# Optimization experiments

Hardware: AMD Instinct MI355X
Metric: run time of the kernel (lower is better)

Reference implementation:

```python
import jax, jax.numpy as jnp
import numpy as np

B, NPG, C, DEG, DE = 64, 1024, 512, 32, 16  # graphs, nodes/graph, feat dim, avg degree, edge-feat dim
N = B * NPG
E = N * DEG
RATIO = 0.5


def setup_inputs() -> dict:
    key = jax.random.key(0)
    k1, k2, k3, k4 = jax.random.split(key, 4)
    x = jax.random.normal(k1, (N, C), dtype=jnp.float32)
    # edges drawn within each graph block so batch structure is respected
    local = jax.random.randint(k2, (2, E), 0, NPG, dtype=jnp.int32)
    offsets = jnp.repeat(jnp.arange(B, dtype=jnp.int32) * NPG, NPG * DEG)
    edge_index = local + offsets[None, :]
    edge_attr = jax.random.normal(k3, (E, DE), dtype=jnp.float32)
    batch = jnp.repeat(jnp.arange(B, dtype=jnp.int32), NPG)
    W = jax.random.normal(k4, (C, 1), dtype=jnp.float32) * (1.0 / np.sqrt(C))
    b = jnp.zeros((1,), dtype=jnp.float32)
    return {"x": x, "edge_index": edge_index, "edge_attr": edge_attr, "batch": batch,
            "W": W, "b": b, "num_graphs": B, "nodes_per_graph": NPG}


def _gcn_score(x, edge_index, W, b):
    # PyG GCNConv(in_channels, 1): add self-loops, symmetric D^-1/2 (A+I) D^-1/2 norm
    n = x.shape[0]
    loop = jnp.arange(n, dtype=edge_index.dtype)
    s = jnp.concatenate([edge_index[0], loop])
    d = jnp.concatenate([edge_index[1], loop])
    deg = jnp.zeros((n,), x.dtype).at[d].add(jnp.ones((), x.dtype))  # >= 1 via self loops
    dinv = jax.lax.rsqrt(deg)
    norm = dinv[s] * dinv[d]                       # [E+n]
    h = (x @ W)[:, 0]                               # project first: [n]
    score = jnp.zeros((n,), x.dtype).at[d].add(h[s] * norm) + b[0]
    return score


def reference(x, edge_index, edge_attr, batch, W, b, num_graphs, nodes_per_graph):
    n = x.shape[0]
    k = int(np.ceil(RATIO * nodes_per_graph))
    score = _gcn_score(x, edge_index, W, b)         # [n]
    # per-graph top-k (equal-sized graphs -> fixed-shape top_k over [B, NPG])
    sc = score.reshape(num_graphs, nodes_per_graph)
    _, topi = jax.lax.top_k(sc, k)                  # [B, k], score-descending per graph
    offs = (jnp.arange(num_graphs, dtype=edge_index.dtype) * nodes_per_graph)[:, None]
    perm = (topi.astype(edge_index.dtype) + offs).reshape(-1)  # [B*k]
    x_new = x[perm] * jnp.tanh(score[perm])[:, None]
    batch_new = batch[perm]
    # filter_adj: keep edges with both endpoints selected, remap to new ids.
    # Fixed-shape version: full-length edge list with invalid entries = -1 plus a mask.
    sel = jnp.zeros((n,), bool).at[perm].set(True)
    newidx = jnp.full((n,), -1, edge_index.dtype).at[perm].set(
        jnp.arange(perm.shape[0], dtype=edge_index.dtype))
    src, dst = edge_index[0], edge_index[1]
    edge_mask = sel[src] & sel[dst]                 # [E]
    ei_new = jnp.where(edge_mask[None, :], jnp.stack([newidx[src], newidx[dst]]), -1)
    ea_new = jnp.where(edge_mask[:, None], edge_attr, jnp.zeros((), edge_attr.dtype))
    return x_new, ei_new, ea_new, edge_mask, batch_new, perm
```

## Files before the change

### kernel.cpp

```cpp
#include <hip/hip_runtime.h>
#include <math.h>

#define N_NODES 65536
#define C_DIM   512
#define E_EDGES 2097152
#define DE_DIM  16
#define B_GR    64
#define NPG     1024
#define DEG     32
#define EPG     (NPG * DEG)
#define K_SEL   512
#define NK      (B_GR * K_SEL)

#define OUT_XNEW  0
#define OUT_EI    (NK * C_DIM)
#define OUT_EA    (OUT_EI + 2 * E_EDGES)
#define OUT_MASK  (OUT_EA + (size_t)E_EDGES * DE_DIM)
#define OUT_BATCH (OUT_MASK + E_EDGES)
#define OUT_PERM  (OUT_BATCH + NK)

__global__ void k_proj(const float* __restrict__ x,
                       const float* __restrict__ W,
                       float* __restrict__ h,
                       int*   __restrict__ newidx) {
    __shared__ float sW[C_DIM];
    const int t = threadIdx.x;
    ((float2*)sW)[t] = ((const float2*)W)[t];
    __syncthreads();

    const int wave = t >> 6, lane = t & 63;
    const int node = blockIdx.x * 4 + wave;
    const float* xr = x + (size_t)node * C_DIM + lane * 8;
    float4 a0 = ((const float4*)xr)[0];
    float4 a1 = ((const float4*)xr)[1];
    const float* wr = sW + lane * 8;
    float s = a0.x * wr[0] + a0.y * wr[1] + a0.z * wr[2] + a0.w * wr[3]
            + a1.x * wr[4] + a1.y * wr[5] + a1.z * wr[6] + a1.w * wr[7];
#pragma unroll
    for (int off = 32; off > 0; off >>= 1) s += __shfl_down(s, off, 64);
    if (lane == 0) h[node] = s;

    const int gid = blockIdx.x * 256 + t;
    if (gid < N_NODES) newidx[gid] = -1;
}

__global__ void __launch_bounds__(1024)
k_score_topk(const int* __restrict__ src,
             const int* __restrict__ dst,
             const float* __restrict__ h,
             const float* __restrict__ b,
             int*   __restrict__ newidx,
             int*   __restrict__ permw,
             float* __restrict__ mult,
             float* __restrict__ out_perm,
             float* __restrict__ out_batch) {
    __shared__ float hs[NPG];
    __shared__ float dg[NPG];
    __shared__ float sc[NPG];
    __shared__ unsigned long long keys[NPG];

    const int g = blockIdx.x, t = threadIdx.x;
    const int ebase = g * EPG;
    const int nbase = g * NPG;

    hs[t] = h[nbase + t];
    dg[t] = 0.0f;
    sc[t] = 0.0f;
    __syncthreads();

    const int4* dst4 = (const int4*)(dst + ebase);
#pragma unroll
    for (int it = 0; it < EPG / 4096; ++it) {
        int4 d4 = dst4[it * 1024 + t];
        atomicAdd(&dg[d4.x & (NPG - 1)], 1.0f);
        atomicAdd(&dg[d4.y & (NPG - 1)], 1.0f);
        atomicAdd(&dg[d4.z & (NPG - 1)], 1.0f);
        atomicAdd(&dg[d4.w & (NPG - 1)], 1.0f);
    }
    __syncthreads();
    dg[t] = rsqrtf(dg[t] + 1.0f);
    __syncthreads();

    const int4* src4 = (const int4*)(src + ebase);
#pragma unroll
    for (int it = 0; it < EPG / 4096; ++it) {
        int4 s4 = src4[it * 1024 + t];
        int4 d4 = dst4[it * 1024 + t];
        int s0 = s4.x & (NPG - 1), d0 = d4.x & (NPG - 1);
        int s1 = s4.y & (NPG - 1), d1 = d4.y & (NPG - 1);
        int s2 = s4.z & (NPG - 1), d2 = d4.z & (NPG - 1);
        int s3 = s4.w & (NPG - 1), d3 = d4.w & (NPG - 1);
        atomicAdd(&sc[d0], hs[s0] * dg[s0] * dg[d0]);
        atomicAdd(&sc[d1], hs[s1] * dg[s1] * dg[d1]);
        atomicAdd(&sc[d2], hs[s2] * dg[s2] * dg[d2]);
        atomicAdd(&sc[d3], hs[s3] * dg[s3] * dg[d3]);
    }
    __syncthreads();

    {
        const float scf = sc[t] + hs[t] * dg[t] * dg[t] + b[0];
        sc[t] = scf;
        const unsigned int bits = __float_as_uint(scf);
        const unsigned int u = bits ^ ((bits & 0x80000000u) ? 0xFFFFFFFFu : 0x80000000u);
        keys[t] = ((unsigned long long)(~u) << 32) | (unsigned int)t;
    }
    __syncthreads();

    for (int k = 2; k <= NPG; k <<= 1) {
        for (int j = k >> 1; j > 0; j >>= 1) {
            if (t < NPG / 2) {
                const int i = ((t & ~(j - 1)) << 1) | (t & (j - 1));
                const int p = i | j;
                const bool asc = (i & k) == 0;
                const unsigned long long a = keys[i], bb = keys[p];
                if ((a > bb) == asc) { keys[i] = bb; keys[p] = a; }
            }
            __syncthreads();
        }
    }

    if (t < K_SEL) {
        const int li   = (int)(keys[t] & 0xFFFFFFFFull);
        const int node = nbase + li;
        const int j    = g * K_SEL + t;
        permw[j]     = node;
        newidx[node] = j;
        mult[j]      = tanhf(sc[li]);
        out_perm[j]  = (float)node;
        out_batch[j] = (float)g;
    }
}

__global__ void k_xnew(const float* __restrict__ x,
                       const float* __restrict__ mult,
                       const int* __restrict__ permw,
                       float* __restrict__ out) {
    const int row = blockIdx.x * 2 + (threadIdx.x >> 7);
    const int c   = (threadIdx.x & 127) * 4;
    const int node = permw[row];
    const float tt = mult[row];
    float4 v = *(const float4*)(x + (size_t)node * C_DIM + c);
    v.x *= tt; v.y *= tt; v.z *= tt; v.w *= tt;
    *(float4*)(out + (size_t)row * C_DIM + c) = v;
}

__global__ void k_edges(const int* __restrict__ src,
                        const int* __restrict__ dst,
                        const float* __restrict__ ea,
                        const int* __restrict__ newidx,
                        float* __restrict__ out_ei,
                        float* __restrict__ out_ea,
                        float* __restrict__ out_mask) {
    const int gid = blockIdx.x * 256 + threadIdx.x;
    const int e = gid >> 2, c = gid & 3;
    if (e >= E_EDGES) return;
    const int s = src[e], d = dst[e];
    const int ns = newidx[s], nd = newidx[d];
    const bool m = (ns >= 0) && (nd >= 0);

    float4 v = make_float4(0.f, 0.f, 0.f, 0.f);
    if (m) v = ((const float4*)ea)[(size_t)e * 4 + c];
    ((float4*)out_ea)[(size_t)e * 4 + c] = v;

    if (c == 0) {
        out_ei[e]           = m ? (float)ns : -1.0f;
        out_ei[E_EDGES + e] = m ? (float)nd : -1.0f;
        out_mask[e]         = m ? 1.0f : 0.0f;
    }
}

extern "C" void kernel_launch(void* const* d_in, const int* in_sizes, int n_in,
                              void* d_out, int out_size, void* d_ws, size_t ws_size,
                              hipStream_t stream) {
    const float* x    = (const float*)d_in[0];
    const int*   ei   = (const int*)d_in[1];
    const float* ea   = (const float*)d_in[2];
    const float* W    = (const float*)d_in[4];
    const float* b    = (const float*)d_in[5];
    const int* src = ei;
    const int* dst = ei + E_EDGES;

    float* out = (float*)d_out;

    float* h      = (float*)d_ws;
    int*   newidx = (int*)(h + N_NODES);
    int*   permw  = newidx + N_NODES;
    float* mult   = (float*)(permw + NK);

    k_proj<<<N_NODES / 4, 256, 0, stream>>>(x, W, h, newidx);
    k_score_topk<<<B_GR, 1024, 0, stream>>>(src, dst, h, b, newidx, permw, mult,
                                            out + OUT_PERM, out + OUT_BATCH);
    k_xnew<<<NK / 2, 256, 0, stream>>>(x, mult, permw, out + OUT_XNEW);
    k_edges<<<(E_EDGES * 4) / 256, 256, 0, stream>>>(src, dst, ea, newidx,
                                                     out + OUT_EI, out + OUT_EA,
                                                     out + OUT_MASK);
}
```

Measured before the change: 516.2 us.

## Split per-graph degree and score scatter across four blocks per graph; merge tail kernels

The single 64-block score/top-k kernel is split into three kernels. Degree counting and score scattering each run with four blocks per graph, accumulating privately in shared memory and then adding into global arrays with atomics. A separate kernel then does the sort. The x_new gather and the edge-filter kernels are also merged into one launch, so both kinds of work share the GPU. This targets low occupancy in the old 64-block kernel, at the cost of extra launches and global atomics.

```diff
diff --git a/kernel.cpp b/kernel.cpp
--- a/kernel.cpp
+++ b/kernel.cpp
@@ -9,6 +9,8 @@
 #define NPG     1024
 #define DEG     32
 #define EPG     (NPG * DEG)
+#define PARTS   4
+#define EPP     (EPG / PARTS)
 #define K_SEL   512
 #define NK      (B_GR * K_SEL)
 
@@ -22,6 +24,8 @@
 __global__ void k_proj(const float* __restrict__ x,
                        const float* __restrict__ W,
                        float* __restrict__ h,
+                       float* __restrict__ score,
+                       float* __restrict__ deg,
                        int*   __restrict__ newidx) {
     __shared__ float sW[C_DIM];
     const int t = threadIdx.x;
@@ -41,65 +45,98 @@
     if (lane == 0) h[node] = s;
 
     const int gid = blockIdx.x * 256 + t;
-    if (gid < N_NODES) newidx[gid] = -1;
+    if (gid < N_NODES) {
+        score[gid]  = 0.0f;
+        deg[gid]    = 1.0f;
+        newidx[gid] = -1;
+    }
 }
 
 __global__ void __launch_bounds__(1024)
-k_score_topk(const int* __restrict__ src,
-             const int* __restrict__ dst,
-             const float* __restrict__ h,
-             const float* __restrict__ b,
-             int*   __restrict__ newidx,
-             int*   __restrict__ permw,
-             float* __restrict__ mult,
-             float* __restrict__ out_perm,
-             float* __restrict__ out_batch) {
+k_deg_part(const int* __restrict__ dst, float* __restrict__ deg) {
+    __shared__ float dgp[NPG];
+    const int bg = blockIdx.x;
+    const int g = bg >> 2, part = bg & 3;
+    const int t = threadIdx.x;
+    dgp[t] = 0.0f;
+    __syncthreads();
+
+    const int4* d4 = (const int4*)(dst + g * EPG + part * EPP);
+    int4 a = d4[t], b = d4[1024 + t];
+    atomicAdd(&dgp[a.x & (NPG - 1)], 1.0f);
+    atomicAdd(&dgp[a.y & (NPG - 1)], 1.0f);
+    atomicAdd(&dgp[a.z & (NPG - 1)], 1.0f);
+    atomicAdd(&dgp[a.w & (NPG - 1)], 1.0f);
+    atomicAdd(&dgp[b.x & (NPG - 1)], 1.0f);
+    atomicAdd(&dgp[b.y & (NPG - 1)], 1.0f);
+    atomicAdd(&dgp[b.z & (NPG - 1)], 1.0f);
+    atomicAdd(&dgp[b.w & (NPG - 1)], 1.0f);
+    __syncthreads();
+
+    atomicAdd(&deg[g * NPG + t], dgp[t]);
+}
+
+__global__ void __launch_bounds__(1024)
+k_score_part(const int* __restrict__ src, const int* __restrict__ dst,
+             const float* __restrict__ h, const float* __restrict__ deg,
+             float* __restrict__ score) {
     __shared__ float hs[NPG];
-    __shared__ float dg[NPG];
-    __shared__ float sc[NPG];
+    __shared__ float di[NPG];
+    __shared__ float scp[NPG];
+    const int bg = blockIdx.x;
+    const int g = bg >> 2, part = bg & 3;
+    const int t = threadIdx.x;
+    const int nbase = g * NPG;
+
+    hs[t]  = h[nbase + t];
+    di[t]  = rsqrtf(deg[nbase + t]);
+    scp[t] = 0.0f;
+    __syncthreads();
+
+    const int4* s4 = (const int4*)(src + g * EPG + part * EPP);
+    const int4* d4 = (const int4*)(dst + g * EPG + part * EPP);
+    int4 sa = s4[t], sb = s4[1024 + t];
+    int4 da = d4[t], db = d4[1024 + t];
+    {
+        int s0 = sa.x & (NPG-1), d0 = da.x & (NPG-1);
+        int s1 = sa.y & (NPG-1), d1 = da.y & (NPG-1);
+        int s2 = sa.z & (NPG-1), d2 = da.z & (NPG-1);
+        int s3 = sa.w & (NPG-1), d3 = da.w & (NPG-1);
+        atomicAdd(&scp[d0], hs[s0] * di[s0] * di[d0]);
+        atomicAdd(&scp[d1], hs[s1] * di[s1] * di[d1]);
+        atomicAdd(&scp[d2], hs[s2] * di[s2] * di[d2]);
+        atomicAdd(&scp[d3], hs[s3] * di[s3] * di[d3]);
+    }
+    {
+        int s0 = sb.x & (NPG-1), d0 = db.x & (NPG-1);
+        int s1 = sb.y & (NPG-1), d1 = db.y & (NPG-1);
+        int s2 = sb.z & (NPG-1), d2 = db.z & (NPG-1);
+        int s3 = sb.w & (NPG-1), d3 = db.w & (NPG-1);
+        atomicAdd(&scp[d0], hs[s0] * di[s0] * di[d0]);
+        atomicAdd(&scp[d1], hs[s1] * di[s1] * di[d1]);
+        atomicAdd(&scp[d2], hs[s2] * di[s2] * di[d2]);
+        atomicAdd(&scp[d3], hs[s3] * di[s3] * di[d3]);
+    }
+    __syncthreads();
+
+    atomicAdd(&score[nbase + t], scp[t]);
+}
+
+__global__ void __launch_bounds__(1024)
+k_topk(const float* __restrict__ score, const float* __restrict__ h,
+       const float* __restrict__ deg, const float* __restrict__ b,
+       int*   __restrict__ newidx, int* __restrict__ permw,
+       float* __restrict__ mult,
+       float* __restrict__ out_perm, float* __restrict__ out_batch) {
+    __shared__ float scs[NPG];
     __shared__ unsigned long long keys[NPG];
-
     const int g = blockIdx.x, t = threadIdx.x;
-    const int ebase = g * EPG;
     const int nbase = g * NPG;
 
-    hs[t] = h[nbase + t];
-    dg[t] = 0.0f;
-    sc[t] = 0.0f;
-    __syncthreads();
-
-    const int4* dst4 = (const int4*)(dst + ebase);
-#pragma unroll
-    for (int it = 0; it < EPG / 4096; ++it) {
-        int4 d4 = dst4[it * 1024 + t];
-        atomicAdd(&dg[d4.x & (NPG - 1)], 1.0f);
-        atomicAdd(&dg[d4.y & (NPG - 1)], 1.0f);
-        atomicAdd(&dg[d4.z & (NPG - 1)], 1.0f);
-        atomicAdd(&dg[d4.w & (NPG - 1)], 1.0f);
-    }
-    __syncthreads();
-    dg[t] = rsqrtf(dg[t] + 1.0f);
-    __syncthreads();
-
-    const int4* src4 = (const int4*)(src + ebase);
-#pragma unroll
-    for (int it = 0; it < EPG / 4096; ++it) {
-        int4 s4 = src4[it * 1024 + t];
-        int4 d4 = dst4[it * 1024 + t];
-        int s0 = s4.x & (NPG - 1), d0 = d4.x & (NPG - 1);
-        int s1 = s4.y & (NPG - 1), d1 = d4.y & (NPG - 1);
-        int s2 = s4.z & (NPG - 1), d2 = d4.z & (NPG - 1);
-        int s3 = s4.w & (NPG - 1), d3 = d4.w & (NPG - 1);
-        atomicAdd(&sc[d0], hs[s0] * dg[s0] * dg[d0]);
-        atomicAdd(&sc[d1], hs[s1] * dg[s1] * dg[d1]);
-        atomicAdd(&sc[d2], hs[s2] * dg[s2] * dg[d2]);
-        atomicAdd(&sc[d3], hs[s3] * dg[s3] * dg[d3]);
-    }
-    __syncthreads();
-
     {
-        const float scf = sc[t] + hs[t] * dg[t] * dg[t] + b[0];
-        sc[t] = scf;
+        const float dv  = rsqrtf(deg[nbase + t]);
+        const float scf = score[nbase + t] + h[nbase + t] * dv * dv + b[0];
+        scs[t] = scf;
         const unsigned int bits = __float_as_uint(scf);
         const unsigned int u = bits ^ ((bits & 0x80000000u) ? 0xFFFFFFFFu : 0x80000000u);
         keys[t] = ((unsigned long long)(~u) << 32) | (unsigned int)t;
@@ -125,73 +162,82 @@
         const int j    = g * K_SEL + t;
         permw[j]     = node;
         newidx[node] = j;
-        mult[j]      = tanhf(sc[li]);
+        mult[j]      = tanhf(scs[li]);
         out_perm[j]  = (float)node;
         out_batch[j] = (float)g;
     }
 }
 
-__global__ void k_xnew(const float* __restrict__ x,
+#define EDGE_BLKS (E_EDGES / 64)
+#define XNEW_BLKS (NK / 2)
+
+__global__ void k_tail(const float* __restrict__ x,
                        const float* __restrict__ mult,
                        const int* __restrict__ permw,
-                       float* __restrict__ out) {
-    const int row = blockIdx.x * 2 + (threadIdx.x >> 7);
-    const int c   = (threadIdx.x & 127) * 4;
-    const int node = permw[row];
-    const float tt = mult[row];
-    float4 v = *(const float4*)(x + (size_t)node * C_DIM + c);
-    v.x *= tt; v.y *= tt; v.z *= tt; v.w *= tt;
-    *(float4*)(out + (size_t)row * C_DIM + c) = v;
-}
-
-__global__ void k_edges(const int* __restrict__ src,
-                        const int* __restrict__ dst,
-                        const float* __restrict__ ea,
-                        const int* __restrict__ newidx,
-                        float* __restrict__ out_ei,
-                        float* __restrict__ out_ea,
-                        float* __restrict__ out_mask) {
-    const int gid = blockIdx.x * 256 + threadIdx.x;
-    const int e = gid >> 2, c = gid & 3;
-    if (e >= E_EDGES) return;
-    const int s = src[e], d = dst[e];
-    const int ns = newidx[s], nd = newidx[d];
-    const bool m = (ns >= 0) && (nd >= 0);
-
-    float4 v = make_float4(0.f, 0.f, 0.f, 0.f);
-    if (m) v = ((const float4*)ea)[(size_t)e * 4 + c];
-    ((float4*)out_ea)[(size_t)e * 4 + c] = v;
-
-    if (c == 0) {
-        out_ei[e]           = m ? (float)ns : -1.0f;
-        out_ei[E_EDGES + e] = m ? (float)nd : -1.0f;
-        out_mask[e]         = m ? 1.0f : 0.0f;
+                       const int* __restrict__ src,
+                       const int* __restrict__ dst,
+                       const float* __restrict__ ea,
+                       const int* __restrict__ newidx,
+                       float* __restrict__ out_xnew,
+                       float* __restrict__ out_ei,
+                       float* __restrict__ out_ea,
+                       float* __restrict__ out_mask) {
+    int bid = blockIdx.x;
+    if (bid < EDGE_BLKS) {
+        const int gid = bid * 256 + threadIdx.x;
+        const int e = gid >> 2, c = gid & 3;
+        const int s = src[e], d = dst[e];
+        const int ns = newidx[s], nd = newidx[d];
+        const bool m = (ns >= 0) && (nd >= 0);
+
+        float4 v = make_float4(0.f, 0.f, 0.f, 0.f);
+        if (m) v = ((const float4*)ea)[(size_t)e * 4 + c];
+        ((float4*)out_ea)[(size_t)e * 4 + c] = v;
+
+        if (c == 0) {
+            out_ei[e]           = m ? (float)ns : -1.0f;
+            out_ei[E_EDGES + e] = m ? (float)nd : -1.0f;
+            out_mask[e]         = m ? 1.0f : 0.0f;
+        }
+    } else {
+        bid -= EDGE_BLKS;
+        const int row = bid * 2 + (threadIdx.x >> 7);
+        const int c   = (threadIdx.x & 127) * 4;
+        const int node = permw[row];
+        const float tt = mult[row];
+        float4 v = *(const float4*)(x + (size_t)node * C_DIM + c);
+        v.x *= tt; v.y *= tt; v.z *= tt; v.w *= tt;
+        *(float4*)(out_xnew + (size_t)row * C_DIM + c) = v;
     }
 }
 
 extern "C" void kernel_launch(void* const* d_in, const int* in_sizes, int n_in,
                               void* d_out, int out_size, void* d_ws, size_t ws_size,
                               hipStream_t stream) {
-    const float* x    = (const float*)d_in[0];
-    const int*   ei   = (const int*)d_in[1];
-    const float* ea   = (const float*)d_in[2];
-    const float* W    = (const float*)d_in[4];
-    const float* b    = (const float*)d_in[5];
+    const float* x  = (const float*)d_in[0];
+    const int*   ei = (const int*)d_in[1];
+    const float* ea = (const float*)d_in[2];
+    const float* W  = (const float*)d_in[4];
+    const float* b  = (const float*)d_in[5];
     const int* src = ei;
     const int* dst = ei + E_EDGES;
 
     float* out = (float*)d_out;
 
     float* h      = (float*)d_ws;
-    int*   newidx = (int*)(h + N_NODES);
+    float* score  = h + N_NODES;
+    float* deg    = score + N_NODES;
+    int*   newidx = (int*)(deg + N_NODES);
     int*   permw  = newidx + N_NODES;
     float* mult   = (float*)(permw + NK);
 
-    k_proj<<<N_NODES / 4, 256, 0, stream>>>(x, W, h, newidx);
-    k_score_topk<<<B_GR, 1024, 0, stream>>>(src, dst, h, b, newidx, permw, mult,
-                                            out + OUT_PERM, out + OUT_BATCH);
-    k_xnew<<<NK / 2, 256, 0, stream>>>(x, mult, permw, out + OUT_XNEW);
-    k_edges<<<(E_EDGES * 4) / 256, 256, 0, stream>>>(src, dst, ea, newidx,
-                                                     out + OUT_EI, out + OUT_EA,
-                                                     out + OUT_MASK);
-}
+    k_proj<<<N_NODES / 4, 256, 0, stream>>>(x, W, h, score, deg, newidx);
+    k_deg_part<<<B_GR * PARTS, 1024, 0, stream>>>(dst, deg);
+    k_score_part<<<B_GR * PARTS, 1024, 0, stream>>>(src, dst, h, deg, score);
+    k_topk<<<B_GR, 1024, 0, stream>>>(score, h, deg, b, newidx, permw, mult,
+                                      out + OUT_PERM, out + OUT_BATCH);
+    k_tail<<<EDGE_BLKS + XNEW_BLKS, 256, 0, stream>>>(x, mult, permw, src, dst, ea,
+                                                      newidx, out + OUT_XNEW,
+                                                      out + OUT_EI, out + OUT_EA,
+                                                      out + OUT_MASK);
+}
```

Result: faster. 460.9 us (-10.7%).
